# Kernel optimization log

Measured on AMD Instinct MI355X. Metric: run time of the kernel, lower is better.

Reference implementation:

```python
import jax, jax.numpy as jnp
import numpy as np

N_CELL = 66
N_SUB = 29934
N = N_CELL + N_SUB  # 30000 nodes
F = 256
E_HALF = 480000
K = 3
LAYERS = 2
BN_EPS = 1e-5


def setup_inputs() -> dict:
    key = jax.random.key(0)
    ks = jax.random.split(key, 8)
    cell_feat = jax.random.normal(ks[0], (N_CELL, F), dtype=jnp.float32)
    sub_feat = jax.random.normal(ks[1], (N_SUB, F), dtype=jnp.float32)
    # interaction_edge builds a symmetric directed edge list: (a,b) and (b,a)
    src = jax.random.randint(ks[2], (E_HALF,), 0, N)
    dst = jax.random.randint(ks[3], (E_HALF,), 0, N)
    edge_index = jnp.stack([jnp.concatenate([src, dst]),
                            jnp.concatenate([dst, src])], axis=0)
    ew_half = jax.random.uniform(ks[4], (E_HALF,), dtype=jnp.float32, minval=0.1, maxval=1.0)
    edge_weight = jnp.concatenate([ew_half, ew_half])
    glorot = np.sqrt(6.0 / (F + F))
    W1 = jax.random.uniform(ks[5], (F, F), dtype=jnp.float32, minval=-glorot, maxval=glorot)
    W2 = jax.random.uniform(ks[6], (F, F), dtype=jnp.float32, minval=-glorot, maxval=glorot)
    b1 = jnp.zeros((F,), jnp.float32)
    b2 = jnp.zeros((F,), jnp.float32)
    prelu_w = jnp.full((F,), 0.25, jnp.float32)  # PReLU default init
    gamma = jnp.ones((F,), jnp.float32)
    beta = jnp.zeros((F,), jnp.float32)
    return {"cell_feat": cell_feat, "sub_feat": sub_feat,
            "edge_index": edge_index, "edge_weight": edge_weight,
            "W1": W1, "b1": b1, "W2": W2, "b2": b2,
            "prelu_w": prelu_w, "gamma": gamma, "beta": beta}


def _gcn_norm(edge_index, edge_weight, n):
    # SGConv's gcn_norm: add self-loops (weight 1), symmetric degree normalization
    loop = jnp.arange(n)
    row = jnp.concatenate([edge_index[0], loop])  # source j
    col = jnp.concatenate([edge_index[1], loop])  # target i
    ew = jnp.concatenate([edge_weight, jnp.ones((n,), edge_weight.dtype)])
    deg = jax.ops.segment_sum(ew, col, num_segments=n)
    dinv = jnp.where(deg > 0, jax.lax.rsqrt(deg), 0.0)
    norm = dinv[row] * ew * dinv[col]
    return row, col, norm


def _sgconv(x, row, col, norm, W, b, n):
    # K-hop propagation: x <- A_hat^K x, then linear
    for _ in range(K):
        x = jax.ops.segment_sum(norm[:, None] * x[row], col, num_segments=n)
    return x @ W.T + b


def _prelu_bn(x, prelu_w, gamma, beta):
    x = jnp.where(x >= 0, x, prelu_w * x)
    mean = jnp.mean(x, axis=0)
    var = jnp.mean(jnp.square(x - mean), axis=0)  # biased, training-mode BN
    return gamma * (x - mean) * jax.lax.rsqrt(var + BN_EPS) + beta


def reference(cell_feat, sub_feat, edge_index, edge_weight,
              W1, b1, W2, b2, prelu_w, gamma, beta):
    x = jnp.concatenate([cell_feat, sub_feat], axis=0)  # [N, F]
    n = x.shape[0]
    row, col, norm = _gcn_norm(edge_index, edge_weight, n)
    for W, b in ((W1, b1), (W2, b2)):
        x = _sgconv(x, row, col, norm, W, b, n)
        x = _prelu_bn(x, prelu_w, gamma, beta)
    return x[:N_CELL, :], x[N_CELL:, :]
```

## Files before the change

### kernel.cpp

```cpp
#include <hip/hip_runtime.h>
#include <hip/hip_bf16.h>

constexpr int NN    = 30000;
constexpr int NCELL = 66;
constexpr int NF    = 256;
constexpr int CAP   = 80;
constexpr float EPS = 1e-5f;

using bf16x8 = __attribute__((ext_vector_type(8))) short;
using f32x4  = __attribute__((ext_vector_type(4))) float;

__device__ __forceinline__ float bf2f(unsigned short u) {
    return __uint_as_float(((unsigned)u) << 16);
}
__device__ __forceinline__ unsigned short f2bf(float f) {
    __hip_bfloat16 h = __float2bfloat16(f);
    return *reinterpret_cast<unsigned short*>(&h);
}
__device__ __forceinline__ void acc8(float* acc, float4 u, float w) {
    unsigned a = __float_as_uint(u.x), b = __float_as_uint(u.y);
    unsigned c = __float_as_uint(u.z), d = __float_as_uint(u.w);
    acc[0] += w * __uint_as_float(a << 16);
    acc[1] += w * __uint_as_float(a & 0xffff0000u);
    acc[2] += w * __uint_as_float(b << 16);
    acc[3] += w * __uint_as_float(b & 0xffff0000u);
    acc[4] += w * __uint_as_float(c << 16);
    acc[5] += w * __uint_as_float(c & 0xffff0000u);
    acc[6] += w * __uint_as_float(d << 16);
    acc[7] += w * __uint_as_float(d & 0xffff0000u);
}
__device__ __forceinline__ void edge_meta(const unsigned* p, int& r, float& w) {
    unsigned v = *p;
    r = (int)(v & 0xffffu);
    w = (float)(v >> 16) * (1.0f / 65536.0f);
}

__global__ void k_init(int* fill, float* sums) {
    int i = blockIdx.x * 256 + threadIdx.x;
    if (i < NN) fill[i] = 0;
    if (i < 2 * NF) sums[i] = 0.0f;
}

__global__ void k_zero_stats(float* sums) {
    int i = threadIdx.x;
    if (i < 2 * NF) sums[i] = 0.0f;
}

__global__ void k_cvtw(const float4* __restrict__ W, ushort4* __restrict__ Wh) {
    int idx = blockIdx.x * 256 + threadIdx.x;
    if (idx >= NF * NF / 4) return;
    float4 v = W[idx];
    ushort4 o;
    o.x = f2bf(v.x); o.y = f2bf(v.y); o.z = f2bf(v.z); o.w = f2bf(v.w);
    Wh[idx] = o;
}

__global__ void k_scatter(const int* __restrict__ ei, const float* __restrict__ ew,
                          int* fill, unsigned* __restrict__ bkt, int E) {
    int e = blockIdx.x * 256 + threadIdx.x;
    if (e >= E) return;
    int row = ei[e];
    int col = ei[E + e];
    unsigned q = (unsigned)(ew[e] * 65536.0f);
    int pos = atomicAdd(&fill[col], 1);
    unsigned v = ((unsigned)row) | (q << 16);
    __builtin_nontemporal_store(v, &bkt[(size_t)col * CAP + pos]);
}

__global__ void k_deg(const unsigned* __restrict__ bkt, const int* __restrict__ fill,
                      float* __restrict__ s1, float* __restrict__ s2) {
    int i = blockIdx.x * 256 + threadIdx.x;
    if (i >= NN) return;
    int cnt = fill[i];
    unsigned sq = 0;
    const unsigned* p = bkt + (size_t)i * CAP;
    for (int e = 0; e < cnt; e++) sq += (p[e] >> 16);
    float deg = 1.0f + (float)sq * (1.0f / 65536.0f);
    float di = rsqrtf(deg);
    s2[i] = di;
    s1[i] = di * di;
}

__global__ void k_concat_h(const float4* __restrict__ cell, const float4* __restrict__ sub,
                           const float* __restrict__ dinv, ushort4* __restrict__ xh) {
    int idx = blockIdx.x * 256 + threadIdx.x;
    if (idx >= NN * (NF / 4)) return;
    const int CELL4 = NCELL * (NF / 4);
    float4 v = (idx < CELL4) ? cell[idx] : sub[idx - CELL4];
    float di = dinv[idx >> 6];
    ushort4 o;
    o.x = f2bf(v.x * di); o.y = f2bf(v.y * di);
    o.z = f2bf(v.z * di); o.w = f2bf(v.w * di);
    xh[idx] = o;
}

__global__ __launch_bounds__(256) void k_prop(const ushort* __restrict__ xin,
                                              ushort* __restrict__ xout,
                                              const int* __restrict__ fill,
                                              const unsigned* __restrict__ bkt,
                                              const float* __restrict__ scale) {
    int n = blockIdx.x * 4 + (threadIdx.x >> 6);
    int lane = threadIdx.x & 63;
    int half = lane >> 5;
    int fb = lane & 31;
    const float4* xrow = (const float4*)xin;
    const unsigned* base = bkt + (size_t)n * CAP;
    int cnt = fill[n];
    float acc[8];
    #pragma unroll
    for (int i = 0; i < 8; i++) acc[i] = 0.f;
    int steps = cnt >> 1;
    int it = 0;
    int e = half;
    for (; it + 8 <= steps; it += 8, e += 16) {
        int r0, r1, r2, r3, r4, r5, r6, r7;
        float w0, w1, w2, w3, w4, w5, w6, w7;
        edge_meta(base + e,      r0, w0);
        edge_meta(base + e + 2,  r1, w1);
        edge_meta(base + e + 4,  r2, w2);
        edge_meta(base + e + 6,  r3, w3);
        edge_meta(base + e + 8,  r4, w4);
        edge_meta(base + e + 10, r5, w5);
        edge_meta(base + e + 12, r6, w6);
        edge_meta(base + e + 14, r7, w7);
        float4 u0 = xrow[r0 * 32 + fb];
        float4 u1 = xrow[r1 * 32 + fb];
        float4 u2 = xrow[r2 * 32 + fb];
        float4 u3 = xrow[r3 * 32 + fb];
        float4 u4 = xrow[r4 * 32 + fb];
        float4 u5 = xrow[r5 * 32 + fb];
        float4 u6 = xrow[r6 * 32 + fb];
        float4 u7 = xrow[r7 * 32 + fb];
        acc8(acc, u0, w0); acc8(acc, u1, w1); acc8(acc, u2, w2); acc8(acc, u3, w3);
        acc8(acc, u4, w4); acc8(acc, u5, w5); acc8(acc, u6, w6); acc8(acc, u7, w7);
    }
    for (; it + 4 <= steps; it += 4, e += 8) {
        int r0, r1, r2, r3; float w0, w1, w2, w3;
        edge_meta(base + e,     r0, w0);
        edge_meta(base + e + 2, r1, w1);
        edge_meta(base + e + 4, r2, w2);
        edge_meta(base + e + 6, r3, w3);
        float4 u0 = xrow[r0 * 32 + fb];
        float4 u1 = xrow[r1 * 32 + fb];
        float4 u2 = xrow[r2 * 32 + fb];
        float4 u3 = xrow[r3 * 32 + fb];
        acc8(acc, u0, w0); acc8(acc, u1, w1); acc8(acc, u2, w2); acc8(acc, u3, w3);
    }
    for (; it < steps; ++it, e += 2) {
        int r0; float w0;
        edge_meta(base + e, r0, w0);
        float4 u0 = xrow[r0 * 32 + fb];
        acc8(acc, u0, w0);
    }
    if ((cnt & 1) && half == 0) {
        int r0; float w0;
        edge_meta(base + cnt - 1, r0, w0);
        float4 u0 = xrow[r0 * 32 + fb];
        acc8(acc, u0, w0);
    }
    #pragma unroll
    for (int i = 0; i < 8; i++) acc[i] += __shfl_xor(acc[i], 32);
    if (half == 0) {
        float4 u = xrow[n * 32 + fb];
        acc8(acc, u, 1.0f);
        float sc = scale[n];
        #pragma unroll
        for (int i = 0; i < 8; i++) acc[i] *= sc;
        unsigned p0 = ((unsigned)f2bf(acc[1]) << 16) | f2bf(acc[0]);
        unsigned p1 = ((unsigned)f2bf(acc[3]) << 16) | f2bf(acc[2]);
        unsigned p2 = ((unsigned)f2bf(acc[5]) << 16) | f2bf(acc[4]);
        unsigned p3 = ((unsigned)f2bf(acc[7]) << 16) | f2bf(acc[6]);
        float4 o;
        o.x = __uint_as_float(p0); o.y = __uint_as_float(p1);
        o.z = __uint_as_float(p2); o.w = __uint_as_float(p3);
        ((float4*)xout)[n * 32 + fb] = o;
    }
}

__global__ __launch_bounds__(256) void k_gemm_fused(const short* __restrict__ A,
                                                    const short* __restrict__ B,
                                                    const float* __restrict__ bias,
                                                    const float* __restrict__ pw,
                                                    float* __restrict__ y,
                                                    float* __restrict__ sums) {
    constexpr int RT = NN / 16;
    int w    = threadIdx.x >> 6;
    int lane = threadIdx.x & 63;
    int rt   = blockIdx.x * 4 + w;
    int ml   = lane & 15;
    int q    = lane >> 4;
    bool valid = rt < RT;
    __shared__ float red[2][4][NF];
    f32x4 acc[16];
    #pragma unroll
    for (int i = 0; i < 16; i++) acc[i] = (f32x4){0.f, 0.f, 0.f, 0.f};
    if (valid) {
        const short* arow = A + (rt * 16 + ml) * NF + q * 8;
        #pragma unroll
        for (int ks = 0; ks < 8; ks++) {
            bf16x8 a = *(const bf16x8*)(arow + ks * 32);
            #pragma unroll
            for (int nt = 0; nt < 16; nt++) {
                bf16x8 b = *(const bf16x8*)(B + (nt * 16 + ml) * NF + ks * 32 + q * 8);
                acc[nt] = __builtin_amdgcn_mfma_f32_16x16x32_bf16(a, b, acc[nt], 0, 0, 0);
            }
        }
    }
    #pragma unroll
    for (int nt = 0; nt < 16; nt++) {
        int col = nt * 16 + ml;
        float s = 0.f, s2 = 0.f;
        if (valid) {
            float bb = bias[col];
            float pc = pw[col];
            #pragma unroll
            for (int r = 0; r < 4; r++) {
                float v = acc[nt][r] + bb;
                v = (v >= 0.f) ? v : pc * v;
                s += v; s2 += v * v;
                y[(rt * 16 + q * 4 + r) * NF + col] = v;
            }
        }
        s  += __shfl_xor(s, 16);  s  += __shfl_xor(s, 32);
        s2 += __shfl_xor(s2, 16); s2 += __shfl_xor(s2, 32);
        if (lane < 16) { red[0][w][col] = s; red[1][w][col] = s2; }
    }
    __syncthreads();
    int t = threadIdx.x;
    float v0 = red[0][0][t] + red[0][1][t] + red[0][2][t] + red[0][3][t];
    float v1 = red[1][0][t] + red[1][1][t] + red[1][2][t] + red[1][3][t];
    atomicAdd(&sums[t], v0);
    atomicAdd(&sums[NF + t], v1);
}

__global__ void k_finalize(const float* __restrict__ sums, const float* __restrict__ gamma,
                           const float* __restrict__ beta, float* __restrict__ ss) {
    int t = threadIdx.x;
    float mean = sums[t] / (float)NN;
    float var = sums[NF + t] / (float)NN - mean * mean;
    if (var < 0.f) var = 0.f;
    float istd = rsqrtf(var + EPS);
    float sc = gamma[t] * istd;
    ss[t] = sc;
    ss[NF + t] = beta[t] - mean * sc;
}

__global__ void k_apply_h(const float4* __restrict__ y, const float* __restrict__ ss,
                          const float* __restrict__ dinv, ushort4* __restrict__ xh) {
    int idx = blockIdx.x * 256 + threadIdx.x;
    if (idx >= NN * (NF / 4)) return;
    int f = (idx & 63) * 4;
    float di = dinv[idx >> 6];
    float4 v = y[idx];
    ushort4 o;
    o.x = f2bf((v.x * ss[f]     + ss[NF + f])     * di);
    o.y = f2bf((v.y * ss[f + 1] + ss[NF + f + 1]) * di);
    o.z = f2bf((v.z * ss[f + 2] + ss[NF + f + 2]) * di);
    o.w = f2bf((v.w * ss[f + 3] + ss[NF + f + 3]) * di);
    xh[idx] = o;
}

__global__ void k_apply_out(const float4* __restrict__ y, const float* __restrict__ ss,
                            float4* __restrict__ out) {
    int idx = blockIdx.x * 256 + threadIdx.x;
    if (idx >= NN * (NF / 4)) return;
    int f = (idx & 63) * 4;
    float4 v = y[idx];
    float4 o;
    o.x = v.x * ss[f]     + ss[NF + f];
    o.y = v.y * ss[f + 1] + ss[NF + f + 1];
    o.z = v.z * ss[f + 2] + ss[NF + f + 2];
    o.w = v.w * ss[f + 3] + ss[NF + f + 3];
    out[idx] = o;
}

extern "C" void kernel_launch(void* const* d_in, const int* in_sizes, int n_in,
                              void* d_out, int out_size, void* d_ws, size_t ws_size,
                              hipStream_t stream) {
    const float* cell  = (const float*)d_in[0];
    const float* sub   = (const float*)d_in[1];
    const int*   ei    = (const int*)  d_in[2];
    const float* ew    = (const float*)d_in[3];
    const float* W1    = (const float*)d_in[4];
    const float* bias1 = (const float*)d_in[5];
    const float* W2    = (const float*)d_in[6];
    const float* bias2 = (const float*)d_in[7];
    const float* pw    = (const float*)d_in[8];
    const float* gamma = (const float*)d_in[9];
    const float* beta  = (const float*)d_in[10];
    float* out = (float*)d_out;
    const int E = in_sizes[3];

    char* ws = (char*)d_ws;
    size_t off = 0;
    auto alloc = [&](size_t bytes) -> void* {
        void* p = ws + off;
        off = (off + bytes + 255) & ~((size_t)255);
        return p;
    };
    ushort*   xh0  = (ushort*)  alloc((size_t)NN * NF * 2);
    ushort*   xh1  = (ushort*)  alloc((size_t)NN * NF * 2);
    float*    yf   = (float*)   alloc((size_t)NN * NF * 4);
    ushort*   W1h  = (ushort*)  alloc((size_t)NF * NF * 2);
    ushort*   W2h  = (ushort*)  alloc((size_t)NF * NF * 2);
    unsigned* bkt  = (unsigned*)alloc((size_t)NN * CAP * 4);
    int*      fill = (int*)     alloc((size_t)NN * 4);
    float*    s1   = (float*)   alloc((size_t)NN * 4);
    float*    s2   = (float*)   alloc((size_t)NN * 4);
    float*    sums = (float*)   alloc((size_t)2 * NF * 4);
    float*    ss   = (float*)   alloc((size_t)2 * NF * 4);

    const int gN  = (NN + 255) / 256;
    const int gE  = (E + 255) / 256;
    const int gV4 = (NN * NF / 4 + 255) / 256;
    const int gW4 = (NF * NF / 4 + 255) / 256;
    const int gP  = NN / 4;
    const int gG  = (NN / 16 + 3) / 4;

    k_init<<<gN, 256, 0, stream>>>(fill, sums);
    k_cvtw<<<gW4, 256, 0, stream>>>((const float4*)W1, (ushort4*)W1h);
    k_cvtw<<<gW4, 256, 0, stream>>>((const float4*)W2, (ushort4*)W2h);
    k_scatter<<<gE, 256, 0, stream>>>(ei, ew, fill, bkt, E);
    k_deg<<<gN, 256, 0, stream>>>(bkt, fill, s1, s2);
    k_concat_h<<<gV4, 256, 0, stream>>>((const float4*)cell, (const float4*)sub, s2, (ushort4*)xh0);

    k_prop<<<gP, 256, 0, stream>>>(xh0, xh1, fill, bkt, s1);
    k_prop<<<gP, 256, 0, stream>>>(xh1, xh0, fill, bkt, s1);
    k_prop<<<gP, 256, 0, stream>>>(xh0, xh1, fill, bkt, s2);
    k_gemm_fused<<<gG, 256, 0, stream>>>((const short*)xh1, (const short*)W1h, bias1, pw, yf, sums);
    k_finalize<<<1, 256, 0, stream>>>(sums, gamma, beta, ss);
    k_apply_h<<<gV4, 256, 0, stream>>>((const float4*)yf, ss, s2, (ushort4*)xh0);
    k_zero_stats<<<1, 512, 0, stream>>>(sums);

    k_prop<<<gP, 256, 0, stream>>>(xh0, xh1, fill, bkt, s1);
    k_prop<<<gP, 256, 0, stream>>>(xh1, xh0, fill, bkt, s1);
    k_prop<<<gP, 256, 0, stream>>>(xh0, xh1, fill, bkt, s2);
    k_gemm_fused<<<gG, 256, 0, stream>>>((const short*)xh1, (const short*)W2h, bias2, pw, yf, sums);
    k_finalize<<<1, 256, 0, stream>>>(sums, gamma, beta, ss);
    k_apply_out<<<gV4, 256, 0, stream>>>((const float4*)yf, ss, (float4*)out);
}
```

Measured before the change: 655.0 us.

## Split propagation into feature chunks mapped to XCD pairs for L2 locality

The propagation kernel now splits the 256 features into four 64-feature chunks. Blocks are mapped so each pair of XCDs (from blockIdx & 7) handles one chunk, meaning each XCD's L2 only caches a quarter of the feature matrix. Within a wave, 8 edge groups × 8 lanes each load 128-byte segments, then reduce across lanes with shuffles. Edge metadata loads and output stores use nontemporal hints. The grid is four times larger, and the extra reductions and redundant metadata reads across chunks are added cost.

```diff
diff --git a/kernel.cpp b/kernel.cpp
--- a/kernel.cpp
+++ b/kernel.cpp
@@ -31,6 +31,11 @@
 }
 __device__ __forceinline__ void edge_meta(const unsigned* p, int& r, float& w) {
     unsigned v = *p;
+    r = (int)(v & 0xffffu);
+    w = (float)(v >> 16) * (1.0f / 65536.0f);
+}
+__device__ __forceinline__ void edge_meta_nt(const unsigned* p, int& r, float& w) {
+    unsigned v = __builtin_nontemporal_load(p);
     r = (int)(v & 0xffffu);
     w = (float)(v >> 16) * (1.0f / 65536.0f);
 }
@@ -99,69 +104,43 @@
                                               const int* __restrict__ fill,
                                               const unsigned* __restrict__ bkt,
                                               const float* __restrict__ scale) {
-    int n = blockIdx.x * 4 + (threadIdx.x >> 6);
+    int b    = blockIdx.x;
+    int xcd  = b & 7;
+    int c    = xcd >> 1;
+    int idx  = (b >> 3) * 2 + (xcd & 1);
+    int n    = idx * 4 + (threadIdx.x >> 6);
     int lane = threadIdx.x & 63;
-    int half = lane >> 5;
-    int fb = lane & 31;
-    const float4* xrow = (const float4*)xin;
+    int eg   = lane >> 3;
+    int f    = lane & 7;
+    const float4* xl = (const float4*)xin + c * 8 + f;
     const unsigned* base = bkt + (size_t)n * CAP;
     int cnt = fill[n];
     float acc[8];
     #pragma unroll
     for (int i = 0; i < 8; i++) acc[i] = 0.f;
-    int steps = cnt >> 1;
-    int it = 0;
-    int e = half;
-    for (; it + 8 <= steps; it += 8, e += 16) {
-        int r0, r1, r2, r3, r4, r5, r6, r7;
-        float w0, w1, w2, w3, w4, w5, w6, w7;
-        edge_meta(base + e,      r0, w0);
-        edge_meta(base + e + 2,  r1, w1);
-        edge_meta(base + e + 4,  r2, w2);
-        edge_meta(base + e + 6,  r3, w3);
-        edge_meta(base + e + 8,  r4, w4);
-        edge_meta(base + e + 10, r5, w5);
-        edge_meta(base + e + 12, r6, w6);
-        edge_meta(base + e + 14, r7, w7);
-        float4 u0 = xrow[r0 * 32 + fb];
-        float4 u1 = xrow[r1 * 32 + fb];
-        float4 u2 = xrow[r2 * 32 + fb];
-        float4 u3 = xrow[r3 * 32 + fb];
-        float4 u4 = xrow[r4 * 32 + fb];
-        float4 u5 = xrow[r5 * 32 + fb];
-        float4 u6 = xrow[r6 * 32 + fb];
-        float4 u7 = xrow[r7 * 32 + fb];
-        acc8(acc, u0, w0); acc8(acc, u1, w1); acc8(acc, u2, w2); acc8(acc, u3, w3);
-        acc8(acc, u4, w4); acc8(acc, u5, w5); acc8(acc, u6, w6); acc8(acc, u7, w7);
-    }
-    for (; it + 4 <= steps; it += 4, e += 8) {
-        int r0, r1, r2, r3; float w0, w1, w2, w3;
-        edge_meta(base + e,     r0, w0);
-        edge_meta(base + e + 2, r1, w1);
-        edge_meta(base + e + 4, r2, w2);
-        edge_meta(base + e + 6, r3, w3);
-        float4 u0 = xrow[r0 * 32 + fb];
-        float4 u1 = xrow[r1 * 32 + fb];
-        float4 u2 = xrow[r2 * 32 + fb];
-        float4 u3 = xrow[r3 * 32 + fb];
-        acc8(acc, u0, w0); acc8(acc, u1, w1); acc8(acc, u2, w2); acc8(acc, u3, w3);
-    }
-    for (; it < steps; ++it, e += 2) {
-        int r0; float w0;
-        edge_meta(base + e, r0, w0);
-        float4 u0 = xrow[r0 * 32 + fb];
-        acc8(acc, u0, w0);
-    }
-    if ((cnt & 1) && half == 0) {
-        int r0; float w0;
-        edge_meta(base + cnt - 1, r0, w0);
-        float4 u0 = xrow[r0 * 32 + fb];
-        acc8(acc, u0, w0);
+    for (int e0 = 0; e0 < cnt; e0 += 32) {
+        int e = e0 + eg;
+        int r0 = 0, r1 = 0, r2 = 0, r3 = 0;
+        float w0 = 0.f, w1 = 0.f, w2 = 0.f, w3 = 0.f;
+        if (e < cnt)      edge_meta_nt(base + e,      r0, w0);
+        if (e + 8 < cnt)  edge_meta_nt(base + e + 8,  r1, w1);
+        if (e + 16 < cnt) edge_meta_nt(base + e + 16, r2, w2);
+        if (e + 24 < cnt) edge_meta_nt(base + e + 24, r3, w3);
+        float4 u0 = xl[r0 * 32];
+        float4 u1 = xl[r1 * 32];
+        float4 u2 = xl[r2 * 32];
+        float4 u3 = xl[r3 * 32];
+        acc8(acc, u0, w0); acc8(acc, u1, w1);
+        acc8(acc, u2, w2); acc8(acc, u3, w3);
     }
     #pragma unroll
-    for (int i = 0; i < 8; i++) acc[i] += __shfl_xor(acc[i], 32);
-    if (half == 0) {
-        float4 u = xrow[n * 32 + fb];
+    for (int i = 0; i < 8; i++) {
+        acc[i] += __shfl_xor(acc[i], 8);
+        acc[i] += __shfl_xor(acc[i], 16);
+        acc[i] += __shfl_xor(acc[i], 32);
+    }
+    if (eg == 0) {
+        float4 u = xl[n * 32];
         acc8(acc, u, 1.0f);
         float sc = scale[n];
         #pragma unroll
@@ -170,10 +149,10 @@
         unsigned p1 = ((unsigned)f2bf(acc[3]) << 16) | f2bf(acc[2]);
         unsigned p2 = ((unsigned)f2bf(acc[5]) << 16) | f2bf(acc[4]);
         unsigned p3 = ((unsigned)f2bf(acc[7]) << 16) | f2bf(acc[6]);
-        float4 o;
-        o.x = __uint_as_float(p0); o.y = __uint_as_float(p1);
-        o.z = __uint_as_float(p2); o.w = __uint_as_float(p3);
-        ((float4*)xout)[n * 32 + fb] = o;
+        f32x4 o;
+        o[0] = __uint_as_float(p0); o[1] = __uint_as_float(p1);
+        o[2] = __uint_as_float(p2); o[3] = __uint_as_float(p3);
+        __builtin_nontemporal_store(o, (f32x4*)xout + n * 32 + c * 8 + f);
     }
 }
 
@@ -314,7 +293,7 @@
     const int gE  = (E + 255) / 256;
     const int gV4 = (NN * NF / 4 + 255) / 256;
     const int gW4 = (NF * NF / 4 + 255) / 256;
-    const int gP  = NN / 4;
+    const int gP  = NN;
     const int gG  = (NN / 16 + 3) / 4;
 
     k_init<<<gN, 256, 0, stream>>>(fill, sums);
```

Measured after the change: 796.4 us. 1.22x slower.
